# Performance work log

Hardware: AMD Instinct MI355X
Metric: run time of the kernel (lower is better)

Reference implementation:

```python
import jax, jax.numpy as jnp
import numpy as np

D_MODEL = 1024
N_HEADS = 16
EPS = 1e-6


def setup_inputs() -> dict:
    key = jax.random.key(0)
    k1, k2, k3 = jax.random.split(key, 3)
    B, T, D = 2, 2048, D_MODEL
    x = jax.random.normal(k1, (B, T, D), dtype=jnp.float32)
    # learned params
    norm_weight = jnp.ones((D,), dtype=jnp.float32)
    qkv_w = jax.random.normal(k2, (3 * D, D), dtype=jnp.float32) * (1.0 / np.sqrt(D))
    out_w = jax.random.normal(k3, (D, D), dtype=jnp.float32) * (1.0 / np.sqrt(D))
    return {"x": x, "norm_weight": norm_weight, "qkv_w": qkv_w, "out_w": out_w}


def reference(x, norm_weight, qkv_w, out_w):
    B, T, D = x.shape
    H = N_HEADS
    d = D // H
    # RMSNorm
    ms = jnp.mean(x * x, axis=-1, keepdims=True)
    xn = x * jax.lax.rsqrt(ms + EPS) * norm_weight
    # QKV projection (Linear, no bias): y = x @ W^T
    qkv = jnp.einsum('btd,ed->bte', xn, qkv_w)  # (B,T,3D)
    q, k, v = jnp.split(qkv, 3, axis=-1)
    q = q.reshape(B, T, H, d)
    k = k.reshape(B, T, H, d)
    v = v.reshape(B, T, H, d)
    # scores (B,H,T,T) with causal mask
    scores = jnp.einsum('bqhd,bkhd->bhqk', q, k) / np.sqrt(d).astype(np.float32)
    causal = jnp.tril(jnp.ones((T, T), dtype=bool))
    scores = jnp.where(causal[None, None], scores, -jnp.inf)
    probs = jax.nn.softmax(scores, axis=-1)
    ctx = jnp.einsum('bhqk,bkhd->bqhd', probs, v)  # (B,T,H,d)
    out = ctx.reshape(B, T, D)
    out = jnp.einsum('btd,ed->bte', out, out_w)
    return out
```

## Files before the change

kernel.cpp:

```cpp
#include <hip/hip_runtime.h>
#include <stdint.h>

#define B_SZ 2
#define T_SZ 2048
#define DMODEL 1024
#define HCNT 16
#define HD 64
#define MROWS (B_SZ * T_SZ)

typedef __attribute__((ext_vector_type(8))) __bf16 bf16x8;
typedef __attribute__((ext_vector_type(4))) __bf16 bf16x4;
typedef __attribute__((ext_vector_type(4))) float f32x4;
typedef __attribute__((ext_vector_type(8))) unsigned short u16x8;

__device__ __forceinline__ unsigned short f2bf(float f) {
  union { float f; uint32_t u; } v; v.f = f;
  uint32_t u = v.u;
  u += 0x7fffu + ((u >> 16) & 1u);
  return (unsigned short)(u >> 16);
}

__device__ __forceinline__ float fexp2(float x) {
#if __has_builtin(__builtin_amdgcn_exp2f)
  return __builtin_amdgcn_exp2f(x);
#else
  return exp2f(x);
#endif
}

__device__ __forceinline__ void gld_lds16(const void* g, void* l) {
  __builtin_amdgcn_global_load_lds((__attribute__((address_space(1))) void*)(uintptr_t)g,
                                   (__attribute__((address_space(3))) void*)l, 16, 0, 0);
}

__global__ __launch_bounds__(256)
void cvt_all(const float* __restrict__ qkv_w, const float* __restrict__ out_w,
             unsigned short* __restrict__ dst) {
  int i = blockIdx.x * 256 + threadIdx.x;
  const int n1 = 3 * DMODEL * DMODEL / 4;
  float4 v = (i < n1) ? ((const float4*)qkv_w)[i] : ((const float4*)out_w)[i - n1];
  ushort4 o;
  o.x = f2bf(v.x); o.y = f2bf(v.y); o.z = f2bf(v.z); o.w = f2bf(v.w);
  ((ushort4*)dst)[i] = o;
}

__global__ __launch_bounds__(256)
void rmsnorm_bf16(const float* __restrict__ x, const float* __restrict__ w,
                  unsigned short* __restrict__ xn) {
  const int row = blockIdx.x;
  const int t = threadIdx.x;
  float4 v = ((const float4*)(x + (size_t)row * DMODEL))[t];
  float ss = v.x * v.x + v.y * v.y + v.z * v.z + v.w * v.w;
#pragma unroll
  for (int o = 1; o < 64; o <<= 1) ss += __shfl_xor(ss, o, 64);
  __shared__ float red[4];
  if ((t & 63) == 0) red[t >> 6] = ss;
  __syncthreads();
  float tot = red[0] + red[1] + red[2] + red[3];
  float scale = rsqrtf(tot * (1.0f / (float)DMODEL) + 1e-6f);
  float4 wv = ((const float4*)w)[t];
  ushort4 o;
  o.x = f2bf(v.x * scale * wv.x);
  o.y = f2bf(v.y * scale * wv.y);
  o.z = f2bf(v.z * scale * wv.z);
  o.w = f2bf(v.w * scale * wv.w);
  ((ushort4*)(xn + (size_t)row * DMODEL))[t] = o;
}

__device__ __forceinline__ void stage128x64(const unsigned short* g, int ldg,
                                            unsigned short* lds, int tid) {
  const int wave = tid >> 6;
#pragma unroll
  for (int i = 0; i < 4; ++i) {
    int row = i * 32 + (tid >> 3);
    const unsigned short* gp = g + (size_t)row * ldg + (((tid & 7) ^ (row & 7)) << 3);
    gld_lds16(gp, lds + i * 2048 + wave * 512);
  }
}

template <int F32OUT>
__global__ __launch_bounds__(256, 2)
void gemm_bt(const unsigned short* __restrict__ A, const unsigned short* __restrict__ B,
             void* __restrict__ Cv, int M, int N, int K, int nbx) {
  __shared__ __align__(16) unsigned short As[2][128 * 64];
  __shared__ __align__(16) unsigned short Bs[2][128 * 64];
  const int t = threadIdx.x, wave = t >> 6, lane = t & 63;
  const int cpx = gridDim.x >> 3;
  const int swz = (blockIdx.x & 7) * cpx + (blockIdx.x >> 3);
  const int m0 = (swz / nbx) * 128, n0 = (swz % nbx) * 128;
  const int wr = wave >> 1, wc = wave & 1;
  const int c = lane & 15, qg = lane >> 4;
  f32x4 acc[4][4] = {};
  const int nk = K >> 6;
  stage128x64(A + (size_t)m0 * K, K, As[0], t);
  stage128x64(B + (size_t)n0 * K, K, Bs[0], t);
  __syncthreads();
  int buf = 0;
  for (int kt = 0; kt < nk; ++kt) {
    if (kt + 1 < nk) {
      stage128x64(A + (size_t)m0 * K + (kt + 1) * 64, K, As[buf ^ 1], t);
      stage128x64(B + (size_t)n0 * K + (kt + 1) * 64, K, Bs[buf ^ 1], t);
    }
#pragma unroll
    for (int kk = 0; kk < 2; ++kk) {
      bf16x8 af[4], bfr[4];
#pragma unroll
      for (int mi = 0; mi < 4; ++mi) {
        int row = wr * 64 + mi * 16 + c;
        af[mi] = *(const bf16x8*)&As[buf][row * 64 + (((kk * 4 + qg) ^ (row & 7)) << 3)];
      }
#pragma unroll
      for (int ni = 0; ni < 4; ++ni) {
        int row = wc * 64 + ni * 16 + c;
        bfr[ni] = *(const bf16x8*)&Bs[buf][row * 64 + (((kk * 4 + qg) ^ (row & 7)) << 3)];
      }
#pragma unroll
      for (int mi = 0; mi < 4; ++mi)
#pragma unroll
        for (int ni = 0; ni < 4; ++ni)
          acc[mi][ni] = __builtin_amdgcn_mfma_f32_16x16x32_bf16(af[mi], bfr[ni], acc[mi][ni], 0, 0, 0);
    }
    __syncthreads();
    buf ^= 1;
  }
  const int cr = qg * 4;
#pragma unroll
  for (int mi = 0; mi < 4; ++mi)
#pragma unroll
    for (int ni = 0; ni < 4; ++ni) {
      int row = m0 + wr * 64 + mi * 16 + cr;
      int col = n0 + wc * 64 + ni * 16 + c;
      if (F32OUT) {
        float* C = (float*)Cv;
#pragma unroll
        for (int r = 0; r < 4; ++r) C[(size_t)(row + r) * N + col] = acc[mi][ni][r];
      } else {
        unsigned short* C = (unsigned short*)Cv;
#pragma unroll
        for (int r = 0; r < 4; ++r) C[(size_t)(row + r) * N + col] = f2bf(acc[mi][ni][r]);
      }
    }
}

__global__ __attribute__((amdgpu_flat_work_group_size(256, 256), amdgpu_waves_per_eu(4, 4)))
void attn_causal(const unsigned short* __restrict__ qkv, unsigned short* __restrict__ ctx) {
  __shared__ __align__(16) unsigned short Ks[128 * 64];
  __shared__ __align__(16) unsigned short Vt[2][64 * 72];
  __shared__ __align__(16) unsigned short Pl[4][16 * 40];
  const int tid = threadIdx.x, wave = tid >> 6, lane = tid & 63;
  const int id = blockIdx.x;
  const int bh = id & 31;
  const int ts = id >> 5;
  const int f = ts & 7, rank = ts >> 3;
  const int qt = (rank == 0) ? (31 - f) : (rank == 1) ? f : (rank == 2) ? (16 + f) : (15 - f);
  const int b = bh >> 4, h = bh & 15;
  const int q0 = qt * 64 + wave * 16;
  const int nit = (qt >> 1) + 1;
  const int c = lane & 15, qg = lane >> 4;
  const size_t base = (size_t)b * T_SZ * 3 * DMODEL;
  const unsigned short* Kg = qkv + base + DMODEL + h * HD;
  const unsigned short* Vg = qkv + base + 2 * DMODEL + h * HD;

  const float QSC = 0.125f * 1.4426950408889634f;
  bf16x8 aq[2];
#pragma unroll
  for (int kk = 0; kk < 2; ++kk) {
    bf16x8 q = *(const bf16x8*)(qkv + base + (size_t)(q0 + c) * 3 * DMODEL + h * HD + kk * 32 + qg * 8);
#pragma unroll
    for (int j = 0; j < 8; ++j) q[j] = (__bf16)((float)q[j] * QSC);
    aq[kk] = q;
  }

  float mst = -3e38f, lst = 0.f;
  f32x4 aco[4];
#pragma unroll
  for (int nd = 0; nd < 4; ++nd)
#pragma unroll
    for (int r = 0; r < 4; ++r) aco[nd][r] = 0.f;

  auto stageK = [&](int kb) {
#pragma unroll
    for (int i = 0; i < 4; ++i) {
      int row = i * 32 + (tid >> 3);
      gld_lds16(Kg + (size_t)(kb + row) * 3 * DMODEL + (((tid & 7) ^ (row & 7)) << 3),
                &Ks[i * 2048 + (wave << 9)]);
    }
  };
  auto loadV = [&](int kb, u16x8* v) {
#pragma unroll
    for (int i = 0; i < 4; ++i)
      v[i] = *(const u16x8*)(Vg + (size_t)(kb + i * 32 + (tid >> 3)) * 3 * DMODEL + (tid & 7) * 8);
  };
  auto writeV = [&](const u16x8* v) {
#pragma unroll
    for (int i = 0; i < 4; ++i) {
      int ch = i >> 1;
      int kv = (i & 1) * 32 + (tid >> 3);
#pragma unroll
      for (int j = 0; j < 8; ++j) {
        int dd = (tid & 7) * 8 + j;
        int ff = (tid & 7) ^ j;
        Vt[ch][dd * 72 + ((((kv >> 3) ^ ff) << 3) | (kv & 7))] = v[i][j];
      }
    }
  };

  u16x8 vn[4];

  auto computeTile = [&](int kb, bool domask, bool hn) {
    f32x4 s[8] = {};
    __builtin_amdgcn_s_setprio(1);
#pragma unroll
    for (int kk = 0; kk < 2; ++kk) {
      bf16x8 bk[8];
#pragma unroll
      for (int ni = 0; ni < 8; ++ni) {
        int row = ni * 16 + c;
        int crd = kk * 4 + qg;
        bk[ni] = *(const bf16x8*)&Ks[row * 64 + ((crd ^ (row & 7)) << 3)];
      }
#pragma unroll
      for (int ni = 0; ni < 8; ++ni)
        s[ni] = __builtin_amdgcn_mfma_f32_16x16x32_bf16(bk[ni], aq[kk], s[ni], 0, 0, 0);
    }
    __builtin_amdgcn_s_setprio(0);
    if (hn) loadV(kb + 128, vn);
    if (domask) {
#pragma unroll
      for (int ni = 0; ni < 8; ++ni)
#pragma unroll
        for (int r = 0; r < 4; ++r) {
          int kg = kb + ni * 16 + qg * 4 + r;
          if (kg > q0 + c) s[ni][r] = -1e30f;
        }
    }
    float rm = -3e38f;
#pragma unroll
    for (int ni = 0; ni < 8; ++ni)
#pragma unroll
      for (int r = 0; r < 4; ++r) rm = fmaxf(rm, s[ni][r]);
    rm = fmaxf(rm, __shfl_xor(rm, 16, 64));
    rm = fmaxf(rm, __shfl_xor(rm, 32, 64));
    float mo = mst, mn = mo;
    if (__any(rm > mo + 11.5f)) {
      mn = fmaxf(mo, rm);
      float corr = fexp2(mo - mn);
      lst *= corr;
      mst = mn;
#pragma unroll
      for (int r = 0; r < 4; ++r) {
        float cr = __shfl(corr, qg * 20 + r, 64);
#pragma unroll
        for (int nd = 0; nd < 4; ++nd) aco[nd][r] *= cr;
      }
    }
    float rs = 0.f;
#pragma unroll
    for (int ni = 0; ni < 8; ++ni)
#pragma unroll
      for (int r = 0; r < 4; ++r) {
        float pv = fexp2(s[ni][r] - mn);
        s[ni][r] = pv;
        rs += pv;
      }
    rs += __shfl_xor(rs, 16, 64);
    rs += __shfl_xor(rs, 32, 64);
    lst += rs;
    unsigned short* P = Pl[wave];
    __builtin_amdgcn_s_setprio(1);
#pragma unroll
    for (int ch = 0; ch < 2; ++ch)
#pragma unroll
      for (int kk = 0; kk < 2; ++kk) {
#pragma unroll
        for (int par = 0; par < 2; ++par) {
          int ni = ch * 4 + kk * 2 + par;
          bf16x4 pk;
#pragma unroll
          for (int r = 0; r < 4; ++r) pk[r] = (__bf16)s[ni][r];
          *(bf16x4*)&P[c * 40 + par * 16 + qg * 4] = pk;
        }
        bf16x8 pa = *(const bf16x8*)&P[c * 40 + qg * 8];
        bf16x8 bv[4];
#pragma unroll
        for (int nd = 0; nd < 4; ++nd) {
          int dd = nd * 16 + c;
          int ff = ((dd >> 3) ^ dd) & 7;
          int crd = kk * 4 + qg;
          bv[nd] = *(const bf16x8*)&Vt[ch][dd * 72 + ((crd ^ ff) << 3)];
        }
#pragma unroll
        for (int nd = 0; nd < 4; ++nd)
          aco[nd] = __builtin_amdgcn_mfma_f32_16x16x32_bf16(pa, bv[nd], aco[nd], 0, 0, 0);
      }
    __builtin_amdgcn_s_setprio(0);
  };

  stageK(0);
  loadV(0, vn);
  writeV(vn);
  __syncthreads();
  for (int t = 0; t < nit; ++t) {
    const int kb = t * 128;
    const bool hn = (t + 1 < nit);
    computeTile(kb, t == nit - 1, hn);
    __syncthreads();
    if (hn) { stageK(kb + 128); writeV(vn); }
    __syncthreads();
  }

  unsigned short* outp = ctx + (size_t)b * T_SZ * DMODEL + h * HD;
  float linv = 1.f / lst;
#pragma unroll
  for (int r = 0; r < 4; ++r) {
    float inv = __shfl(linv, qg * 20 + r, 64);
    int q = q0 + qg * 4 + r;
#pragma unroll
    for (int nd = 0; nd < 4; ++nd)
      outp[(size_t)q * DMODEL + nd * 16 + c] = f2bf(aco[nd][r] * inv);
  }
}

extern "C" void kernel_launch(void* const* d_in, const int* in_sizes, int n_in,
                              void* d_out, int out_size, void* d_ws, size_t ws_size,
                              hipStream_t stream) {
  const float* x = (const float*)d_in[0];
  const float* nw = (const float*)d_in[1];
  const float* qkv_w = (const float*)d_in[2];
  const float* out_w = (const float*)d_in[3];
  float* out = (float*)d_out;

  unsigned short* ws = (unsigned short*)d_ws;
  unsigned short* xn = ws;
  unsigned short* qkvw = xn + (size_t)MROWS * DMODEL;
  unsigned short* outw = qkvw + (size_t)3 * DMODEL * DMODEL;
  unsigned short* qkv = outw + (size_t)DMODEL * DMODEL;
  unsigned short* ctx = qkv + (size_t)MROWS * 3 * DMODEL;

  cvt_all<<<dim3(4096), dim3(256), 0, stream>>>(qkv_w, out_w, qkvw);
  rmsnorm_bf16<<<dim3(MROWS), dim3(256), 0, stream>>>(x, nw, xn);
  gemm_bt<0><<<dim3(768), dim3(256), 0, stream>>>(xn, qkvw, qkv, MROWS, 3 * DMODEL, DMODEL, 24);
  attn_causal<<<dim3(1024), dim3(256), 0, stream>>>(qkv, ctx);
  gemm_bt<1><<<dim3(256), dim3(256), 0, stream>>>(ctx, outw, out, MROWS, DMODEL, DMODEL, 8);
}
```

Measured before the change: 133.2 us.

## Double-buffer K/V tiles and pair causal query tiles per attention block

The attention kernel now double-buffers the K and V LDS tiles so the next tile's loads are issued before the current tile's compute, dropping one barrier per iteration. Each block processes two paired query tiles (15-p and p) in sequence for load balance, halving the grid to 512 blocks. The row-sum is computed with an extra MFMA against a ones vector instead of shuffle reductions, and launch bounds switch to allowing 2 blocks per CU. This doubles LDS use and changes occupancy, and the extra MFMA adds matrix work in exchange for removing VALU and shuffle work.

```diff
diff --git a/kernel.cpp b/kernel.cpp
--- a/kernel.cpp
+++ b/kernel.cpp
@@ -142,48 +142,34 @@
     }
 }
 
-__global__ __attribute__((amdgpu_flat_work_group_size(256, 256), amdgpu_waves_per_eu(4, 4)))
+__global__ __launch_bounds__(256, 2)
 void attn_causal(const unsigned short* __restrict__ qkv, unsigned short* __restrict__ ctx) {
-  __shared__ __align__(16) unsigned short Ks[128 * 64];
-  __shared__ __align__(16) unsigned short Vt[2][64 * 72];
+  __shared__ __align__(16) unsigned short Ks[2][128 * 64];
+  __shared__ __align__(16) unsigned short Vt[2][2][64 * 72];
   __shared__ __align__(16) unsigned short Pl[4][16 * 40];
   const int tid = threadIdx.x, wave = tid >> 6, lane = tid & 63;
   const int id = blockIdx.x;
   const int bh = id & 31;
-  const int ts = id >> 5;
-  const int f = ts & 7, rank = ts >> 3;
-  const int qt = (rank == 0) ? (31 - f) : (rank == 1) ? f : (rank == 2) ? (16 + f) : (15 - f);
+  const int pr = id >> 5;
+  const int p = pr & 7, half = pr >> 3;
   const int b = bh >> 4, h = bh & 15;
-  const int q0 = qt * 64 + wave * 16;
-  const int nit = (qt >> 1) + 1;
   const int c = lane & 15, qg = lane >> 4;
   const size_t base = (size_t)b * T_SZ * 3 * DMODEL;
   const unsigned short* Kg = qkv + base + DMODEL + h * HD;
   const unsigned short* Vg = qkv + base + 2 * DMODEL + h * HD;
+  unsigned short* outp = ctx + (size_t)b * T_SZ * DMODEL + h * HD;
 
   const float QSC = 0.125f * 1.4426950408889634f;
-  bf16x8 aq[2];
-#pragma unroll
-  for (int kk = 0; kk < 2; ++kk) {
-    bf16x8 q = *(const bf16x8*)(qkv + base + (size_t)(q0 + c) * 3 * DMODEL + h * HD + kk * 32 + qg * 8);
-#pragma unroll
-    for (int j = 0; j < 8; ++j) q[j] = (__bf16)((float)q[j] * QSC);
-    aq[kk] = q;
-  }
-
-  float mst = -3e38f, lst = 0.f;
-  f32x4 aco[4];
-#pragma unroll
-  for (int nd = 0; nd < 4; ++nd)
-#pragma unroll
-    for (int r = 0; r < 4; ++r) aco[nd][r] = 0.f;
-
-  auto stageK = [&](int kb) {
+  bf16x8 ones;
+#pragma unroll
+  for (int j = 0; j < 8; ++j) ones[j] = (__bf16)1.0f;
+
+  auto stageK = [&](int kb, int bufi) {
 #pragma unroll
     for (int i = 0; i < 4; ++i) {
       int row = i * 32 + (tid >> 3);
       gld_lds16(Kg + (size_t)(kb + row) * 3 * DMODEL + (((tid & 7) ^ (row & 7)) << 3),
-                &Ks[i * 2048 + (wave << 9)]);
+                &Ks[bufi][i * 2048 + (wave << 9)]);
     }
   };
   auto loadV = [&](int kb, u16x8* v) {
@@ -191,7 +177,7 @@
     for (int i = 0; i < 4; ++i)
       v[i] = *(const u16x8*)(Vg + (size_t)(kb + i * 32 + (tid >> 3)) * 3 * DMODEL + (tid & 7) * 8);
   };
-  auto writeV = [&](const u16x8* v) {
+  auto writeV = [&](int bufi, const u16x8* v) {
 #pragma unroll
     for (int i = 0; i < 4; ++i) {
       int ch = i >> 1;
@@ -200,125 +186,130 @@
       for (int j = 0; j < 8; ++j) {
         int dd = (tid & 7) * 8 + j;
         int ff = (tid & 7) ^ j;
-        Vt[ch][dd * 72 + ((((kv >> 3) ^ ff) << 3) | (kv & 7))] = v[i][j];
+        Vt[bufi][ch][dd * 72 + ((((kv >> 3) ^ ff) << 3) | (kv & 7))] = v[i][j];
       }
     }
   };
 
-  u16x8 vn[4];
-
-  auto computeTile = [&](int kb, bool domask, bool hn) {
-    f32x4 s[8] = {};
-    __builtin_amdgcn_s_setprio(1);
+  auto runPhase = [&](int qt) {
+    const int q0 = qt * 128 + half * 64 + wave * 16;
+    const int nit = qt + 1;
+    bf16x8 aq[2];
 #pragma unroll
     for (int kk = 0; kk < 2; ++kk) {
-      bf16x8 bk[8];
-#pragma unroll
-      for (int ni = 0; ni < 8; ++ni) {
-        int row = ni * 16 + c;
-        int crd = kk * 4 + qg;
-        bk[ni] = *(const bf16x8*)&Ks[row * 64 + ((crd ^ (row & 7)) << 3)];
-      }
+      bf16x8 q = *(const bf16x8*)(qkv + base + (size_t)(q0 + c) * 3 * DMODEL + h * HD + kk * 32 + qg * 8);
+#pragma unroll
+      for (int j = 0; j < 8; ++j) q[j] = (__bf16)((float)q[j] * QSC);
+      aq[kk] = q;
+    }
+    float mst = -3e38f;
+    f32x4 aco[4] = {};
+    f32x4 acs = {};
+    u16x8 vn[4];
+    stageK(0, 0);
+    loadV(0, vn);
+    writeV(0, vn);
+    __syncthreads();
+    int kbuf = 0;
+    for (int t = 0; t < nit; ++t) {
+      const int kb = t * 128;
+      const bool hn = (t + 1 < nit);
+      if (hn) { stageK(kb + 128, kbuf ^ 1); loadV(kb + 128, vn); }
+      f32x4 s[8] = {};
+      __builtin_amdgcn_s_setprio(1);
+#pragma unroll
+      for (int kk = 0; kk < 2; ++kk) {
+        bf16x8 bk[8];
+#pragma unroll
+        for (int ni = 0; ni < 8; ++ni) {
+          int row = ni * 16 + c;
+          int crd = kk * 4 + qg;
+          bk[ni] = *(const bf16x8*)&Ks[kbuf][row * 64 + ((crd ^ (row & 7)) << 3)];
+        }
+#pragma unroll
+        for (int ni = 0; ni < 8; ++ni)
+          s[ni] = __builtin_amdgcn_mfma_f32_16x16x32_bf16(bk[ni], aq[kk], s[ni], 0, 0, 0);
+      }
+      __builtin_amdgcn_s_setprio(0);
+      if (t == nit - 1) {
+#pragma unroll
+        for (int ni = 0; ni < 8; ++ni)
+#pragma unroll
+          for (int r = 0; r < 4; ++r) {
+            int kg = kb + ni * 16 + qg * 4 + r;
+            if (kg > q0 + c) s[ni][r] = -1e30f;
+          }
+      }
+      float rm = -3e38f;
 #pragma unroll
       for (int ni = 0; ni < 8; ++ni)
-        s[ni] = __builtin_amdgcn_mfma_f32_16x16x32_bf16(bk[ni], aq[kk], s[ni], 0, 0, 0);
-    }
-    __builtin_amdgcn_s_setprio(0);
-    if (hn) loadV(kb + 128, vn);
-    if (domask) {
+#pragma unroll
+        for (int r = 0; r < 4; ++r) rm = fmaxf(rm, s[ni][r]);
+      rm = fmaxf(rm, __shfl_xor(rm, 16, 64));
+      rm = fmaxf(rm, __shfl_xor(rm, 32, 64));
+      float mn = mst;
+      if (__any(rm > mst + 11.5f)) {
+        mn = fmaxf(mst, rm);
+        float corr = fexp2(mst - mn);
+        mst = mn;
+#pragma unroll
+        for (int r = 0; r < 4; ++r) {
+          float cr = __shfl(corr, qg * 20 + r, 64);
+          acs[r] *= cr;
+#pragma unroll
+          for (int nd = 0; nd < 4; ++nd) aco[nd][r] *= cr;
+        }
+      }
 #pragma unroll
       for (int ni = 0; ni < 8; ++ni)
 #pragma unroll
-        for (int r = 0; r < 4; ++r) {
-          int kg = kb + ni * 16 + qg * 4 + r;
-          if (kg > q0 + c) s[ni][r] = -1e30f;
+        for (int r = 0; r < 4; ++r) s[ni][r] = fexp2(s[ni][r] - mn);
+      unsigned short* P = Pl[wave];
+      __builtin_amdgcn_s_setprio(1);
+#pragma unroll
+      for (int ch = 0; ch < 2; ++ch)
+#pragma unroll
+        for (int kk = 0; kk < 2; ++kk) {
+#pragma unroll
+          for (int par = 0; par < 2; ++par) {
+            int ni = ch * 4 + kk * 2 + par;
+            bf16x4 pk;
+#pragma unroll
+            for (int r = 0; r < 4; ++r) pk[r] = (__bf16)s[ni][r];
+            *(bf16x4*)&P[c * 40 + par * 16 + qg * 4] = pk;
+          }
+          bf16x8 pa = *(const bf16x8*)&P[c * 40 + qg * 8];
+          bf16x8 bv[4];
+#pragma unroll
+          for (int nd = 0; nd < 4; ++nd) {
+            int dd = nd * 16 + c;
+            int ff = ((dd >> 3) ^ dd) & 7;
+            int crd = kk * 4 + qg;
+            bv[nd] = *(const bf16x8*)&Vt[kbuf][ch][dd * 72 + ((crd ^ ff) << 3)];
+          }
+#pragma unroll
+          for (int nd = 0; nd < 4; ++nd)
+            aco[nd] = __builtin_amdgcn_mfma_f32_16x16x32_bf16(pa, bv[nd], aco[nd], 0, 0, 0);
+          acs = __builtin_amdgcn_mfma_f32_16x16x32_bf16(pa, ones, acs, 0, 0, 0);
         }
-    }
-    float rm = -3e38f;
-#pragma unroll
-    for (int ni = 0; ni < 8; ++ni)
-#pragma unroll
-      for (int r = 0; r < 4; ++r) rm = fmaxf(rm, s[ni][r]);
-    rm = fmaxf(rm, __shfl_xor(rm, 16, 64));
-    rm = fmaxf(rm, __shfl_xor(rm, 32, 64));
-    float mo = mst, mn = mo;
-    if (__any(rm > mo + 11.5f)) {
-      mn = fmaxf(mo, rm);
-      float corr = fexp2(mo - mn);
-      lst *= corr;
-      mst = mn;
-#pragma unroll
-      for (int r = 0; r < 4; ++r) {
-        float cr = __shfl(corr, qg * 20 + r, 64);
-#pragma unroll
-        for (int nd = 0; nd < 4; ++nd) aco[nd][r] *= cr;
-      }
-    }
-    float rs = 0.f;
-#pragma unroll
-    for (int ni = 0; ni < 8; ++ni)
-#pragma unroll
-      for (int r = 0; r < 4; ++r) {
-        float pv = fexp2(s[ni][r] - mn);
-        s[ni][r] = pv;
-        rs += pv;
-      }
-    rs += __shfl_xor(rs, 16, 64);
-    rs += __shfl_xor(rs, 32, 64);
-    lst += rs;
-    unsigned short* P = Pl[wave];
-    __builtin_amdgcn_s_setprio(1);
-#pragma unroll
-    for (int ch = 0; ch < 2; ++ch)
-#pragma unroll
-      for (int kk = 0; kk < 2; ++kk) {
-#pragma unroll
-        for (int par = 0; par < 2; ++par) {
-          int ni = ch * 4 + kk * 2 + par;
-          bf16x4 pk;
-#pragma unroll
-          for (int r = 0; r < 4; ++r) pk[r] = (__bf16)s[ni][r];
-          *(bf16x4*)&P[c * 40 + par * 16 + qg * 4] = pk;
-        }
-        bf16x8 pa = *(const bf16x8*)&P[c * 40 + qg * 8];
-        bf16x8 bv[4];
-#pragma unroll
-        for (int nd = 0; nd < 4; ++nd) {
-          int dd = nd * 16 + c;
-          int ff = ((dd >> 3) ^ dd) & 7;
-          int crd = kk * 4 + qg;
-          bv[nd] = *(const bf16x8*)&Vt[ch][dd * 72 + ((crd ^ ff) << 3)];
-        }
-#pragma unroll
-        for (int nd = 0; nd < 4; ++nd)
-          aco[nd] = __builtin_amdgcn_mfma_f32_16x16x32_bf16(pa, bv[nd], aco[nd], 0, 0, 0);
-      }
-    __builtin_amdgcn_s_setprio(0);
+      __builtin_amdgcn_s_setprio(0);
+      if (hn) writeV(kbuf ^ 1, vn);
+      __syncthreads();
+      kbuf ^= 1;
+    }
+#pragma unroll
+    for (int r = 0; r < 4; ++r) {
+      float inv = 1.f / acs[r];
+      int q = q0 + qg * 4 + r;
+#pragma unroll
+      for (int nd = 0; nd < 4; ++nd)
+        outp[(size_t)q * DMODEL + nd * 16 + c] = f2bf(aco[nd][r] * inv);
+    }
   };
 
-  stageK(0);
-  loadV(0, vn);
-  writeV(vn);
+  runPhase(15 - p);
   __syncthreads();
-  for (int t = 0; t < nit; ++t) {
-    const int kb = t * 128;
-    const bool hn = (t + 1 < nit);
-    computeTile(kb, t == nit - 1, hn);
-    __syncthreads();
-    if (hn) { stageK(kb + 128); writeV(vn); }
-    __syncthreads();
-  }
-
-  unsigned short* outp = ctx + (size_t)b * T_SZ * DMODEL + h * HD;
-  float linv = 1.f / lst;
-#pragma unroll
-  for (int r = 0; r < 4; ++r) {
-    float inv = __shfl(linv, qg * 20 + r, 64);
-    int q = q0 + qg * 4 + r;
-#pragma unroll
-    for (int nd = 0; nd < 4; ++nd)
-      outp[(size_t)q * DMODEL + nd * 16 + c] = f2bf(aco[nd][r] * inv);
-  }
+  runPhase(p);
 }
 
 extern "C" void kernel_launch(void* const* d_in, const int* in_sizes, int n_in,
@@ -340,6 +331,6 @@
   cvt_all<<<dim3(4096), dim3(256), 0, stream>>>(qkv_w, out_w, qkvw);
   rmsnorm_bf16<<<dim3(MROWS), dim3(256), 0, stream>>>(x, nw, xn);
   gemm_bt<0><<<dim3(768), dim3(256), 0, stream>>>(xn, qkvw, qkv, MROWS, 3 * DMODEL, DMODEL, 24);
-  attn_causal<<<dim3(1024), dim3(256), 0, stream>>>(qkv, ctx);
+  attn_causal<<<dim3(512), dim3(256), 0, stream>>>(qkv, ctx);
   gemm_bt<1><<<dim3(256), dim3(256), 0, stream>>>(ctx, outw, out, MROWS, DMODEL, DMODEL, 8);
 }
```

After: 121.8 us. 8.5% less time.
